# Kernel tuning notes

Measured on AMD Instinct MI355X. Metric: run time of the kernel, lower is better.

Reference implementation:

```python
import jax, jax.numpy as jnp
import numpy as np

DN = ('NCHW', 'OIHW', 'NCHW')

def conv2d(x, w, pad):
    return jax.lax.conv_general_dilated(x, w, (1, 1), [(pad, pad), (pad, pad)], dimension_numbers=DN)

def conv_module(x, w, g, b):
    # Conv2d -> BN (inference-mode per-channel affine) -> ReLU
    pad = (w.shape[-1] - 1) // 2
    y = conv2d(x, w, pad)
    return jax.nn.relu(y * g[None, :, None, None] + b[None, :, None, None])

def seq_conv_module(x, w, g, b):
    # x: (T, B, C, H, W) -> apply ConvModule per frame by folding T into batch
    T, B, C, H, W = x.shape
    y = conv_module(x.reshape(T * B, C, H, W), w, g, b)
    return y.reshape(T, B, -1, H, W)

def setup_inputs() -> dict:
    key = jax.random.key(0)
    ks = jax.random.split(key, 32)
    Cin, Ck, Cv, Cout = 1024, 256, 512, 512
    T, B, H, W = 4, 1, 64, 64
    s = 0.02
    d = {}
    d['x'] = jax.random.normal(ks[0], (B, Cin, H, W), jnp.float32)
    d['seq'] = jax.random.normal(ks[1], (T, B, Cin, H, W), jnp.float32)
    def mk_cm(i, cin, cout, k):
        return (jax.random.normal(ks[i], (cout, cin, k, k), jnp.float32) * s,
                jnp.ones((cout,), jnp.float32),
                jnp.zeros((cout,), jnp.float32))
    d['wk1'], d['gk1'], d['bk1'] = mk_cm(2, Cin, Ck, 1)
    d['wk2'], d['gk2'], d['bk2'] = mk_cm(3, Ck, Ck, 3)
    d['wv1'], d['gv1'], d['bv1'] = mk_cm(4, Cin, Cv, 1)
    d['wv2'], d['gv2'], d['bv2'] = mk_cm(5, Cv, Cv, 3)
    d['wqk1'], d['gqk1'], d['bqk1'] = mk_cm(6, Cin, Ck, 1)
    d['wqk2'], d['gqk2'], d['bqk2'] = mk_cm(7, Ck, Ck, 3)
    d['wqv1'], d['gqv1'], d['bqv1'] = mk_cm(8, Cin, Cv, 1)
    d['wqv2'], d['gqv2'], d['bqv2'] = mk_cm(9, Cv, Cv, 3)
    d['wb'], d['gb'], d['bb'] = mk_cm(10, 2 * Cv, Cout, 3)
    return d

def reference(x, seq, wk1, gk1, bk1, wk2, gk2, bk2, wv1, gv1, bv1, wv2, gv2, bv2,
              wqk1, gqk1, bqk1, wqk2, gqk2, bqk2, wqv1, gqv1, bqv1, wqv2, gqv2, bqv2,
              wb, gb, bb):
    # memory key/value convs over the T reference frames
    mk = seq_conv_module(seq_conv_module(seq, wk1, gk1, bk1), wk2, gk2, bk2)  # (T,B,Ck,H,W)
    mv = seq_conv_module(seq_conv_module(seq, wv1, gv1, bv1), wv2, gv2, bv2)  # (T,B,Cv,H,W)
    # query key/value convs on current frame
    qk = conv_module(conv_module(x, wqk1, gqk1, bqk1), wqk2, gqk2, bqk2)      # (B,Ck,H,W)
    qv = conv_module(conv_module(x, wqv1, gqv1, bqv1), wqv2, gqv2, bqv2)      # (B,Cv,H,W)
    T, B, Ck, H, W = mk.shape
    Cv = mv.shape[2]
    mk = jnp.transpose(mk, (1, 2, 0, 3, 4)).reshape(B, Ck, T * H * W)         # (B,Ck,THW)
    mv = jnp.transpose(mv, (1, 2, 0, 3, 4)).reshape(B, Cv, T * H * W)         # (B,Cv,THW)
    qkf = qk.reshape(B, Ck, H * W)                                            # (B,Ck,HW)
    # attention: (B,HW,THW); matmul_norm=False so no 1/sqrt(Ck) scaling
    attn = jax.nn.softmax(jnp.einsum('bcq,bck->bqk', qkf, mk), axis=-1)
    mem = jnp.einsum('bqk,bck->bcq', attn, mv).reshape(B, Cv, H, W)
    out = conv_module(jnp.concatenate([qv, mem], axis=1), wb, gb, bb)
    return out
```

## Files before the change

### kernel.cpp

```cpp
#include <hip/hip_runtime.h>
#include <stdint.h>


typedef short bf16x8 __attribute__((ext_vector_type(8)));
typedef float f32x4  __attribute__((ext_vector_type(4)));
typedef unsigned short u16x4 __attribute__((ext_vector_type(4)));

__device__ __forceinline__ unsigned short f2bf(float f) {
  union { float f; unsigned u; } x; x.f = f;
  unsigned r = x.u + 0x7FFFu + ((x.u >> 16) & 1u);
  return (unsigned short)(r >> 16);
}

typedef const __attribute__((address_space(1))) char* as1cp;
typedef __attribute__((address_space(3))) char* as3p;

__device__ __forceinline__ void gl_lds16(const char* g, char* l) {
  __builtin_amdgcn_global_load_lds((as1cp)g, (as3p)l, 16, 0, 0);
}

enum { EP_CL_BNR = 0, EP_CF_BNR_BF16 = 1, EP_CF_BNR_F32 = 2, EP_EXPSUM = 3,
       EP_PVDIV = 4, EP_PART = 5 };

template<int EP, bool CF, bool CONV3, bool XTILED>
__global__ __launch_bounds__(256) void gemm_k(
    const unsigned short* __restrict__ Wp,
    const unsigned short* __restrict__ Xp,
    int K, int Kc, int Xstride, int Xcoloff, int cin_log2,
    void* __restrict__ Op, int Ostride, int Ocoloff, size_t plane,
    const float* __restrict__ g1, const float* __restrict__ b1,
    const float* __restrict__ g2, const float* __restrict__ b2, int gsplit,
    float* __restrict__ rowsum, const char* __restrict__ zp)
{
  __shared__ short Wt[2][128 * 32];
  __shared__ short Xt[2][128 * 32];
  const int tid = threadIdx.x;
  const int w = tid >> 6;
  const int l = tid & 63;
  const int m0 = blockIdx.y * 128;
  const int n0 = blockIdx.x * 128;
  const int wrow0 = CF ? n0 : m0;
  const int xrow0 = CF ? m0 : n0;

  const int ch0 = w, ch1 = w + 4;
  const int sr0 = ch0 * 16 + (l >> 2);
  const int sr1 = ch1 * 16 + (l >> 2);
  const int kbp = (l & 3) << 4;
  const int kbl0 = kbp ^ ((sr0 & 3) << 4);
  const int kbl1 = kbp ^ ((sr1 & 3) << 4);

  const size_t wrb = (size_t)K * 2;
  const size_t xrb = (size_t)Xstride * 2;

  const int wm = (w >> 1) * 64;
  const int wn = (w & 1) * 64;

  const int k_begin = blockIdx.z * Kc;
  const int k_end = (k_begin + Kc < K) ? (k_begin + Kc) : K;

  auto stage = [&](int b, int k0) {
    int ci0 = k0, kh = 1, kw = 1, dpos = 0;
    if (CONV3) {
      int e = k0 >> cin_log2;
      ci0 = k0 & ((1 << cin_log2) - 1);
      kh = e / 3; kw = e - kh * 3;
      dpos = (kh - 1) * 64 + (kw - 1);
    }
    char* Wl = (char*)&Wt[b][0];
    char* Xl = (char*)&Xt[b][0];
    gl_lds16((const char*)Wp + (size_t)(wrow0 + sr0) * wrb + (size_t)k0 * 2 + kbl0,
             Wl + ch0 * 1024);
    gl_lds16((const char*)Wp + (size_t)(wrow0 + sr1) * wrb + (size_t)k0 * 2 + kbl1,
             Wl + ch1 * 1024);
    const char* xs0;
    const char* xs1;
    if constexpr (XTILED) {
      size_t kslab = (size_t)(k0 >> 5) * ((size_t)Xstride * 64);
      xs0 = (const char*)Xp + kslab + (size_t)(xrow0 + sr0) * 64 + kbl0;
      xs1 = (const char*)Xp + kslab + (size_t)(xrow0 + sr1) * 64 + kbl1;
    } else if constexpr (CONV3) {
      int p = xrow0 + sr0;
      int hw = p & 4095;
      int h2 = (hw >> 6) + kh - 1, w2 = (hw & 63) + kw - 1;
      xs0 = ((unsigned)h2 < 64u && (unsigned)w2 < 64u)
          ? (const char*)Xp + (size_t)(p + dpos) * xrb + (size_t)(Xcoloff + ci0) * 2 + kbl0
          : zp + kbl0;
      p = xrow0 + sr1;
      hw = p & 4095;
      h2 = (hw >> 6) + kh - 1; w2 = (hw & 63) + kw - 1;
      xs1 = ((unsigned)h2 < 64u && (unsigned)w2 < 64u)
          ? (const char*)Xp + (size_t)(p + dpos) * xrb + (size_t)(Xcoloff + ci0) * 2 + kbl1
          : zp + kbl1;
    } else {
      xs0 = (const char*)Xp + (size_t)(xrow0 + sr0) * xrb + (size_t)(Xcoloff + k0) * 2 + kbl0;
      xs1 = (const char*)Xp + (size_t)(xrow0 + sr1) * xrb + (size_t)(Xcoloff + k0) * 2 + kbl1;
    }
    gl_lds16(xs0, Xl + ch0 * 1024);
    gl_lds16(xs1, Xl + ch1 * 1024);
  };

  f32x4 acc[4][4] = {};

  int cur = 0;
  stage(0, k_begin);
  for (int k0 = k_begin; k0 < k_end; k0 += 32) {
    if (k0 + 32 < k_end) {
      stage(cur ^ 1, k0 + 32);
      asm volatile("s_waitcnt vmcnt(4)" ::: "memory");
    } else {
      asm volatile("s_waitcnt vmcnt(0)" ::: "memory");
    }
    __builtin_amdgcn_s_barrier();

    const short* Wb = &Wt[cur][0];
    const short* Xb = &Xt[cur][0];
    const short* At = CF ? Xb : Wb;
    const short* Bt = CF ? Wb : Xb;

    bf16x8 af[4], bfv[4];
#pragma unroll
    for (int i = 0; i < 4; i++) {
      int row = wm + i * 16 + (l & 15);
      int kb = ((l >> 4) << 4) ^ ((row & 3) << 4);
      af[i] = *(const bf16x8*)(At + row * 32 + (kb >> 1));
    }
#pragma unroll
    for (int j = 0; j < 4; j++) {
      int row = wn + j * 16 + (l & 15);
      int kb = ((l >> 4) << 4) ^ ((row & 3) << 4);
      bfv[j] = *(const bf16x8*)(Bt + row * 32 + (kb >> 1));
    }
#pragma unroll
    for (int i = 0; i < 4; i++)
#pragma unroll
      for (int j = 0; j < 4; j++)
        acc[i][j] = __builtin_amdgcn_mfma_f32_16x16x32_bf16(af[i], bfv[j], acc[i][j], 0, 0, 0);

    __builtin_amdgcn_s_barrier();
    cur ^= 1;
  }

  const int col = l & 15;
  const int rb = (l >> 4) << 2;

  if constexpr (EP == EP_PART) {
    float* P = (float*)Op + (size_t)blockIdx.z * plane;
#pragma unroll
    for (int j = 0; j < 4; j++) {
      int gn = n0 + wn + j * 16 + col;
#pragma unroll
      for (int i = 0; i < 4; i++) {
        int gm = m0 + wm + i * 16 + rb;
        *(f32x4*)(P + (size_t)gn * Ostride + gm) = acc[i][j];
      }
    }
  }
  if constexpr (EP == EP_CL_BNR) {
#pragma unroll
    for (int i = 0; i < 4; i++) {
      int gm = m0 + wm + i * 16 + rb;
      const float* gp; const float* bp;
      if (gm < gsplit) { gp = g1 + gm; bp = b1 + gm; }
      else             { gp = g2 + (gm - gsplit); bp = b2 + (gm - gsplit); }
      float G[4], B[4];
#pragma unroll
      for (int r = 0; r < 4; r++) { G[r] = gp[r]; B[r] = bp[r]; }
#pragma unroll
      for (int j = 0; j < 4; j++) {
        int gn = n0 + wn + j * 16 + col;
        f32x4 v = acc[i][j];
        u16x4 o;
#pragma unroll
        for (int r = 0; r < 4; r++) o[r] = f2bf(fmaxf(v[r] * G[r] + B[r], 0.f));
        *(u16x4*)((unsigned short*)Op + (size_t)gn * Ostride + Ocoloff + gm) = o;
      }
    }
  }
  if constexpr (EP == EP_CF_BNR_BF16 || EP == EP_CF_BNR_F32) {
#pragma unroll
    for (int j = 0; j < 4; j++) {
      int gn = n0 + wn + j * 16 + col;
      float G = (gn < gsplit) ? g1[gn] : g2[gn - gsplit];
      float Bv = (gn < gsplit) ? b1[gn] : b2[gn - gsplit];
#pragma unroll
      for (int i = 0; i < 4; i++) {
        int gm = m0 + wm + i * 16 + rb;
        f32x4 v = acc[i][j];
        if constexpr (EP == EP_CF_BNR_F32) {
          f32x4 o;
#pragma unroll
          for (int r = 0; r < 4; r++) o[r] = fmaxf(v[r] * G + Bv, 0.f);
          *(f32x4*)((float*)Op + (size_t)gn * Ostride + Ocoloff + gm) = o;
        } else {
          u16x4 o;
#pragma unroll
          for (int r = 0; r < 4; r++) o[r] = f2bf(fmaxf(v[r] * G + Bv, 0.f));
          *(u16x4*)((unsigned short*)Op + (size_t)gn * Ostride + Ocoloff + gm) = o;
        }
      }
    }
  }
  if constexpr (EP == EP_EXPSUM) {
#pragma unroll
    for (int j = 0; j < 4; j++) {
      int gn = n0 + wn + j * 16 + col;
      float s = 0.f;
#pragma unroll
      for (int i = 0; i < 4; i++) {
        int gm = m0 + wm + i * 16 + rb;
        f32x4 v = acc[i][j];
        u16x4 o;
#pragma unroll
        for (int r = 0; r < 4; r++) { float e = __expf(v[r]); s += e; o[r] = f2bf(e); }
        if (gsplit)
          *(u16x4*)((unsigned short*)Op + (size_t)(gm >> 5) * ((size_t)Ostride * 32)
                    + (size_t)gn * 32 + (gm & 31)) = o;
        else
          *(u16x4*)((unsigned short*)Op + (size_t)gn * Ostride + gm) = o;
      }
      s += __shfl_xor(s, 16);
      s += __shfl_xor(s, 32);
      if (l < 16) atomicAdd(rowsum + gn, s);
    }
  }
  if constexpr (EP == EP_PVDIV) {
#pragma unroll
    for (int j = 0; j < 4; j++) {
      int gn = n0 + wn + j * 16 + col;
      float inv = 1.0f / rowsum[gn];
#pragma unroll
      for (int i = 0; i < 4; i++) {
        int gm = m0 + wm + i * 16 + rb;
        f32x4 v = acc[i][j];
        u16x4 o;
#pragma unroll
        for (int r = 0; r < 4; r++) o[r] = f2bf(v[r] * inv);
        *(u16x4*)((unsigned short*)Op + (size_t)gn * Ostride + Ocoloff + gm) = o;
      }
    }
  }
}

enum { RED_BNR_BF16 = 0, RED_PVDIV = 1, RED_BNR_F32 = 2, RED_BNR_BF16_N = 3 };

template<int MODE>
__global__ __launch_bounds__(256) void reduce_k(
    const float* __restrict__ P, int Z, size_t plane, int Cdim,
    void* __restrict__ out, int Ostride, int Ocoloff,
    const float* __restrict__ g1, const float* __restrict__ b1,
    const float* __restrict__ g2, const float* __restrict__ b2, int gsplit,
    const float* __restrict__ rowsum, int total4)
{
  int t = blockIdx.x * 256 + threadIdx.x;
  if (t >= total4) return;
  size_t base = (size_t)t * 4;
  int n = (int)(base / (size_t)Cdim);
  int c = (int)(base % (size_t)Cdim);
  f32x4 s = *(const f32x4*)(P + base);
  for (int z = 1; z < Z; z++) {
    f32x4 v = *(const f32x4*)(P + (size_t)z * plane + base);
    s += v;
  }
  if constexpr (MODE == RED_BNR_BF16) {
    u16x4 o;
#pragma unroll
    for (int r = 0; r < 4; r++) {
      int ch = c + r;
      float G = (ch < gsplit) ? g1[ch] : g2[ch - gsplit];
      float B = (ch < gsplit) ? b1[ch] : b2[ch - gsplit];
      o[r] = f2bf(fmaxf(s[r] * G + B, 0.f));
    }
    *(u16x4*)((unsigned short*)out + (size_t)n * Ostride + Ocoloff + c) = o;
  }
  if constexpr (MODE == RED_BNR_BF16_N) {
    float G = g1[n], B = b1[n];
    u16x4 o;
#pragma unroll
    for (int r = 0; r < 4; r++) o[r] = f2bf(fmaxf(s[r] * G + B, 0.f));
    *(u16x4*)((unsigned short*)out + (size_t)n * Ostride + Ocoloff + c) = o;
  }
  if constexpr (MODE == RED_PVDIV) {
    float inv = 1.0f / rowsum[n];
    u16x4 o;
#pragma unroll
    for (int r = 0; r < 4; r++) o[r] = f2bf(s[r] * inv);
    *(u16x4*)((unsigned short*)out + (size_t)n * Ostride + Ocoloff + c) = o;
  }
  if constexpr (MODE == RED_BNR_F32) {
    float G = g1[n], B = b1[n];
    f32x4 o;
#pragma unroll
    for (int r = 0; r < 4; r++) o[r] = fmaxf(s[r] * G + B, 0.f);
    *(f32x4*)((float*)out + (size_t)n * Ostride + c) = o;
  }
}

__global__ __launch_bounds__(256) void nchw_to_cl(const float* __restrict__ src,
                                                  unsigned short* __restrict__ dst,
                                                  int C, int P) {
  __shared__ float t[32][33];
  int f = blockIdx.z;
  src += (size_t)f * C * P;
  dst += (size_t)f * C * P;
  int p0 = blockIdx.x * 32, c0 = blockIdx.y * 32;
  int a = threadIdx.x & 31, b = threadIdx.x >> 5;
#pragma unroll
  for (int k = 0; k < 4; k++)
    t[b + 8 * k][a] = src[(size_t)(c0 + b + 8 * k) * P + p0 + a];
  __syncthreads();
#pragma unroll
  for (int k = 0; k < 4; k++)
    dst[(size_t)(p0 + b + 8 * k) * C + c0 + a] = f2bf(t[a][b + 8 * k]);
}

__global__ __launch_bounds__(256) void cvt_bf16(const float* __restrict__ s,
                                                unsigned short* __restrict__ d, int n) {
  int i = blockIdx.x * 256 + threadIdx.x;
  if (i < n) d[i] = f2bf(s[i]);
}

__global__ __launch_bounds__(256) void repack3(const float* __restrict__ s,
                                               unsigned short* __restrict__ d,
                                               int ci_log2, int n) {
  int i = blockIdx.x * 256 + threadIdx.x;
  if (i >= n) return;
  int Ci = 1 << ci_log2;
  int ci = i & (Ci - 1);
  int t = i >> ci_log2;
  int e = t % 9;
  int co = t / 9;
  d[i] = f2bf(s[((size_t)co * Ci + ci) * 9 + e]);
}

__global__ __launch_bounds__(256) void fillf(float* p, float v, int n) {
  int i = blockIdx.x * 256 + threadIdx.x;
  if (i < n) p[i] = v;
}

extern "C" void kernel_launch(void* const* d_in, const int* in_sizes, int n_in,
                              void* d_out, int out_size, void* d_ws, size_t ws_size,
                              hipStream_t stream) {
  (void)in_sizes; (void)n_in;
  const float* x    = (const float*)d_in[0];
  const float* seq  = (const float*)d_in[1];
  const float* wk1  = (const float*)d_in[2];
  const float* gk1  = (const float*)d_in[3];
  const float* bk1  = (const float*)d_in[4];
  const float* wk2  = (const float*)d_in[5];
  const float* gk2  = (const float*)d_in[6];
  const float* bk2  = (const float*)d_in[7];
  const float* wv1  = (const float*)d_in[8];
  const float* gv1  = (const float*)d_in[9];
  const float* bv1  = (const float*)d_in[10];
  const float* wv2  = (const float*)d_in[11];
  const float* gv2  = (const float*)d_in[12];
  const float* bv2  = (const float*)d_in[13];
  const float* wqk1 = (const float*)d_in[14];
  const float* gqk1 = (const float*)d_in[15];
  const float* bqk1 = (const float*)d_in[16];
  const float* wqk2 = (const float*)d_in[17];
  const float* gqk2 = (const float*)d_in[18];
  const float* bqk2 = (const float*)d_in[19];
  const float* wqv1 = (const float*)d_in[20];
  const float* gqv1 = (const float*)d_in[21];
  const float* bqv1 = (const float*)d_in[22];
  const float* wqv2 = (const float*)d_in[23];
  const float* gqv2 = (const float*)d_in[24];
  const float* bqv2 = (const float*)d_in[25];
  const float* wb   = (const float*)d_in[26];
  const float* gb   = (const float*)d_in[27];
  const float* bb   = (const float*)d_in[28];

  char* ws = (char*)d_ws;
  size_t off = 0;
  auto alloc = [&](size_t bytes) { size_t o = off; off += (bytes + 255) & ~(size_t)255; return o; };
  size_t o_zp    = alloc(4096);
  size_t o_rs    = alloc(4096 * 4);
  size_t o_wKV1  = alloc((size_t)768 * 1024 * 2);
  size_t o_wQKV1 = alloc((size_t)768 * 1024 * 2);
  size_t o_wK2   = alloc((size_t)256 * 2304 * 2);
  size_t o_wQK2  = alloc((size_t)256 * 2304 * 2);
  size_t o_wV2   = alloc((size_t)512 * 4608 * 2);
  size_t o_wQV2  = alloc((size_t)512 * 4608 * 2);
  size_t o_wB    = alloc((size_t)512 * 9216 * 2);
  size_t o_mk    = alloc((size_t)16384 * 256 * 2);
  size_t o_mv    = alloc((size_t)512 * 16384 * 2);
  size_t o_qk    = alloc((size_t)4096 * 256 * 2);
  size_t o_qvm   = alloc((size_t)4096 * 1024 * 2);
  size_t o_part  = alloc((size_t)8 * 4096 * 512 * 4);
  size_t o_vol   = off;
  size_t o_xT    = o_vol;
  size_t o_seqT  = o_xT + (size_t)4096 * 1024 * 2;
  size_t o_kv1   = o_seqT + (size_t)4 * 4096 * 1024 * 2;
  size_t o_qkv1  = o_kv1 + (size_t)16384 * 768 * 2;
  size_t end1    = o_qkv1 + (size_t)4096 * 768 * 2;
  size_t o_expS  = o_vol;
  size_t end2    = o_expS + (size_t)4096 * 16384 * 2;
  size_t need    = end1 > end2 ? end1 : end2;

  bool SPLIT = ws_size >= need;
  if (!SPLIT) {
    size_t save = o_part;
    o_vol  = save;
    o_xT   = o_vol;
    o_seqT = o_xT + (size_t)4096 * 1024 * 2;
    o_kv1  = o_seqT + (size_t)4 * 4096 * 1024 * 2;
    o_qkv1 = o_kv1 + (size_t)16384 * 768 * 2;
    end1   = o_qkv1 + (size_t)4096 * 768 * 2;
    o_expS = o_vol;
    end2   = o_expS + (size_t)4096 * 16384 * 2;
    need   = end1 > end2 ? end1 : end2;
    if (ws_size < need) {
      fillf<<<(out_size + 255) / 256, 256, 0, stream>>>((float*)d_out, 12345.0f, out_size);
      return;
    }
  }

  const char* zp = ws + o_zp;
  float* rs = (float*)(ws + o_rs);
  unsigned short* wKV1p  = (unsigned short*)(ws + o_wKV1);
  unsigned short* wQKV1p = (unsigned short*)(ws + o_wQKV1);
  unsigned short* wK2p   = (unsigned short*)(ws + o_wK2);
  unsigned short* wQK2p  = (unsigned short*)(ws + o_wQK2);
  unsigned short* wV2p   = (unsigned short*)(ws + o_wV2);
  unsigned short* wQV2p  = (unsigned short*)(ws + o_wQV2);
  unsigned short* wBp    = (unsigned short*)(ws + o_wB);
  unsigned short* mkp    = (unsigned short*)(ws + o_mk);
  unsigned short* mvp    = (unsigned short*)(ws + o_mv);
  unsigned short* qkp    = (unsigned short*)(ws + o_qk);
  unsigned short* qvmp   = (unsigned short*)(ws + o_qvm);
  float* partp           = (float*)(ws + o_part);
  unsigned short* xTp    = (unsigned short*)(ws + o_xT);
  unsigned short* seqTp  = (unsigned short*)(ws + o_seqT);
  unsigned short* kv1p   = (unsigned short*)(ws + o_kv1);
  unsigned short* qkv1p  = (unsigned short*)(ws + o_qkv1);
  unsigned short* expSp  = (unsigned short*)(ws + o_expS);

  hipMemsetAsync(ws + o_zp, 0, 4096, stream);
  hipMemsetAsync(ws + o_rs, 0, 4096 * 4, stream);

  cvt_bf16<<<(256 * 1024 + 255) / 256, 256, 0, stream>>>(wk1, wKV1p, 256 * 1024);
  cvt_bf16<<<(512 * 1024 + 255) / 256, 256, 0, stream>>>(wv1, wKV1p + 256 * 1024, 512 * 1024);
  cvt_bf16<<<(256 * 1024 + 255) / 256, 256, 0, stream>>>(wqk1, wQKV1p, 256 * 1024);
  cvt_bf16<<<(512 * 1024 + 255) / 256, 256, 0, stream>>>(wqv1, wQKV1p + 256 * 1024, 512 * 1024);
  repack3<<<(256 * 2304 + 255) / 256, 256, 0, stream>>>(wk2, wK2p, 8, 256 * 2304);
  repack3<<<(256 * 2304 + 255) / 256, 256, 0, stream>>>(wqk2, wQK2p, 8, 256 * 2304);
  repack3<<<(512 * 4608 + 255) / 256, 256, 0, stream>>>(wv2, wV2p, 9, 512 * 4608);
  repack3<<<(512 * 4608 + 255) / 256, 256, 0, stream>>>(wqv2, wQV2p, 9, 512 * 4608);
  repack3<<<(512 * 9216 + 255) / 256, 256, 0, stream>>>(wb, wBp, 10, 512 * 9216);

  nchw_to_cl<<<dim3(128, 32, 1), 256, 0, stream>>>(x, xTp, 1024, 4096);
  nchw_to_cl<<<dim3(128, 32, 4), 256, 0, stream>>>(seq, seqTp, 1024, 4096);

  gemm_k<EP_CL_BNR, false, false, false><<<dim3(128, 6), 256, 0, stream>>>(
      wKV1p, seqTp, 1024, 1024, 1024, 0, 0, kv1p, 768, 0, 0,
      gk1, bk1, gv1, bv1, 256, rs, zp);

  if (SPLIT) {
    {
      size_t plane = (size_t)4096 * 768;
      gemm_k<EP_PART, false, false, false><<<dim3(32, 6, 4), 256, 0, stream>>>(
          wQKV1p, xTp, 1024, 256, 1024, 0, 0, partp, 768, 0, plane,
          nullptr, nullptr, nullptr, nullptr, 0, rs, zp);
      int t4 = (int)(plane / 4);
      reduce_k<RED_BNR_BF16><<<(t4 + 255) / 256, 256, 0, stream>>>(
          partp, 4, plane, 768, qkv1p, 768, 0, gqk1, bqk1, gqv1, bqv1, 256, rs, t4);
    }
    {
      size_t plane = (size_t)16384 * 256;
      gemm_k<EP_PART, false, true, false><<<dim3(128, 2, 4), 256, 0, stream>>>(
          wK2p, kv1p, 2304, 576, 768, 0, 8, partp, 256, 0, plane,
          nullptr, nullptr, nullptr, nullptr, 0, rs, zp);
      int t4 = (int)(plane / 4);
      reduce_k<RED_BNR_BF16><<<(t4 + 255) / 256, 256, 0, stream>>>(
          partp, 4, plane, 256, mkp, 256, 0, gk2, bk2, gk2, bk2, 256, rs, t4);
    }
    {
      size_t plane = (size_t)4096 * 256;
      gemm_k<EP_PART, false, true, false><<<dim3(32, 2, 8), 256, 0, stream>>>(
          wQK2p, qkv1p, 2304, 288, 768, 0, 8, partp, 256, 0, plane,
          nullptr, nullptr, nullptr, nullptr, 0, rs, zp);
      int t4 = (int)(plane / 4);
      reduce_k<RED_BNR_BF16><<<(t4 + 255) / 256, 256, 0, stream>>>(
          partp, 8, plane, 256, qkp, 256, 0, gqk2, bqk2, gqk2, bqk2, 256, rs, t4);
    }
    {
      size_t plane = (size_t)4096 * 512;
      gemm_k<EP_PART, false, true, false><<<dim3(32, 4, 8), 256, 0, stream>>>(
          wQV2p, qkv1p, 4608, 576, 768, 256, 9, partp, 512, 0, plane,
          nullptr, nullptr, nullptr, nullptr, 0, rs, zp);
      int t4 = (int)(plane / 4);
      reduce_k<RED_BNR_BF16><<<(t4 + 255) / 256, 256, 0, stream>>>(
          partp, 8, plane, 512, qvmp, 1024, 0, gqv2, bqv2, gqv2, bqv2, 512, rs, t4);
    }
    {
      size_t plane = (size_t)512 * 16384;
      gemm_k<EP_PART, true, true, false><<<dim3(4, 128, 2), 256, 0, stream>>>(
          wV2p, kv1p, 4608, 2304, 768, 256, 9, partp, 16384, 0, plane,
          nullptr, nullptr, nullptr, nullptr, 0, rs, zp);
      int t4 = (int)(plane / 4);
      reduce_k<RED_BNR_BF16_N><<<(t4 + 255) / 256, 256, 0, stream>>>(
          partp, 2, plane, 16384, mvp, 16384, 0, gv2, bv2, nullptr, nullptr, 0, rs, t4);
    }
    gemm_k<EP_EXPSUM, false, false, false><<<dim3(32, 128), 256, 0, stream>>>(
        mkp, qkp, 256, 256, 256, 0, 0, expSp, 4096, 0, 0,
        nullptr, nullptr, nullptr, nullptr, 1, rs, zp);
    {
      size_t plane = (size_t)4096 * 512;
      gemm_k<EP_PART, false, false, true><<<dim3(32, 4, 8), 256, 0, stream>>>(
          mvp, expSp, 16384, 2048, 4096, 0, 0, partp, 512, 0, plane,
          nullptr, nullptr, nullptr, nullptr, 0, rs, zp);
      int t4 = (int)(plane / 4);
      reduce_k<RED_PVDIV><<<(t4 + 255) / 256, 256, 0, stream>>>(
          partp, 8, plane, 512, qvmp, 1024, 512, nullptr, nullptr, nullptr, nullptr, 0, rs, t4);
    }
    {
      size_t plane = (size_t)512 * 4096;
      gemm_k<EP_PART, true, true, false><<<dim3(4, 32, 8), 256, 0, stream>>>(
          wBp, qvmp, 9216, 1152, 1024, 0, 10, partp, 4096, 0, plane,
          nullptr, nullptr, nullptr, nullptr, 0, rs, zp);
      int t4 = (int)(plane / 4);
      reduce_k<RED_BNR_F32><<<(t4 + 255) / 256, 256, 0, stream>>>(
          partp, 8, plane, 4096, (float*)d_out, 4096, 0, gb, bb, gb, bb, 512, rs, t4);
    }
  } else {
    gemm_k<EP_CL_BNR, false, false, false><<<dim3(32, 6), 256, 0, stream>>>(
        wQKV1p, xTp, 1024, 1024, 1024, 0, 0, qkv1p, 768, 0, 0,
        gqk1, bqk1, gqv1, bqv1, 256, rs, zp);
    gemm_k<EP_CL_BNR, false, true, false><<<dim3(128, 2), 256, 0, stream>>>(
        wK2p, kv1p, 2304, 2304, 768, 0, 8, mkp, 256, 0, 0,
        gk2, bk2, gk2, bk2, 256, rs, zp);
    gemm_k<EP_CL_BNR, false, true, false><<<dim3(32, 2), 256, 0, stream>>>(
        wQK2p, qkv1p, 2304, 2304, 768, 0, 8, qkp, 256, 0, 0,
        gqk2, bqk2, gqk2, bqk2, 256, rs, zp);
    gemm_k<EP_CL_BNR, false, true, false><<<dim3(32, 4), 256, 0, stream>>>(
        wQV2p, qkv1p, 4608, 4608, 768, 256, 9, qvmp, 1024, 0, 0,
        gqv2, bqv2, gqv2, bqv2, 512, rs, zp);
    gemm_k<EP_CF_BNR_BF16, true, true, false><<<dim3(4, 128), 256, 0, stream>>>(
        wV2p, kv1p, 4608, 4608, 768, 256, 9, mvp, 16384, 0, 0,
        gv2, bv2, gv2, bv2, 512, rs, zp);
    gemm_k<EP_EXPSUM, false, false, false><<<dim3(32, 128), 256, 0, stream>>>(
        mkp, qkp, 256, 256, 256, 0, 0, expSp, 16384, 0, 0,
        nullptr, nullptr, nullptr, nullptr, 0, rs, zp);
    gemm_k<EP_PVDIV, false, false, false><<<dim3(32, 4), 256, 0, stream>>>(
        mvp, expSp, 16384, 16384, 16384, 0, 0, qvmp, 1024, 512, 0,
        nullptr, nullptr, nullptr, nullptr, 0, rs, zp);
    gemm_k<EP_CF_BNR_F32, true, true, false><<<dim3(4, 32), 256, 0, stream>>>(
        wBp, qvmp, 9216, 9216, 1024, 0, 10, (float*)d_out, 4096, 0, 0,
        gb, bb, gb, bb, 512, rs, zp);
  }
}
```

Before: 625.5 us.

## Add 256x256-tile 512-thread GEMM kernel for the large split-K partial GEMMs

Adds a new gemm256 kernel that uses 256x256 output tiles with 8 waves. It stages the K dimension in two 32-wide halves with double-buffered direct global-to-LDS loads, uses a swizzled LDS layout, and raises wave priority around the MFMA burst. Five of the partial-sum GEMMs (3x3 convs, the PV product, and the final conv) now run on it instead of the 128x128 gemm_k. The goal is more data reuse per LDS load and higher MFMA density. The cost is fewer blocks per launch and higher register pressure from 32 accumulators per thread.

```diff
diff --git a/kernel.cpp b/kernel.cpp
--- a/kernel.cpp
+++ b/kernel.cpp
@@ -17,6 +17,131 @@
 
 __device__ __forceinline__ void gl_lds16(const char* g, char* l) {
   __builtin_amdgcn_global_load_lds((as1cp)g, (as3p)l, 16, 0, 0);
+}
+
+template<bool CF, bool CONV3, bool XTILED>
+__global__ __launch_bounds__(512, 2) void gemm256(
+    const unsigned short* __restrict__ Wp,
+    const unsigned short* __restrict__ Xp,
+    int K, int Kc, int Xstride, int Xcoloff, int cin_log2,
+    float* __restrict__ P, int Mtot, size_t plane,
+    const char* __restrict__ zp)
+{
+  __shared__ short Ap[2][2][8192];
+  __shared__ short Bp[2][2][8192];
+  const int tid = threadIdx.x;
+  const int w = tid >> 6;
+  const int l = tid & 63;
+  const int wm_idx = w >> 2;
+  const int wn_idx = w & 3;
+  const int n0 = blockIdx.x * 256;
+  const int m0 = blockIdx.y * 256;
+  const int wrow0 = CF ? n0 : m0;
+  const int xrow0 = CF ? m0 : n0;
+
+  const int g = (l & 7) ^ (l >> 3);
+  const int grow0 = w * 32 + 2 * (l >> 3) + (g >> 2);
+  const int gc = g & 3;
+
+  auto srcW = [&](int grow, int h, int k0) -> const char* {
+    return (const char*)Wp +
+           (((size_t)(wrow0 + grow)) * K + (size_t)(k0 + h * 32 + gc * 8)) * 2;
+  };
+  auto srcX = [&](int grow, int h, int k0) -> const char* {
+    if constexpr (XTILED) {
+      return (const char*)Xp + (size_t)((k0 + h * 32) >> 5) * ((size_t)Xstride * 64)
+             + (size_t)(xrow0 + grow) * 64 + gc * 16;
+    } else if constexpr (CONV3) {
+      int e = k0 >> cin_log2;
+      int ci0 = k0 & ((1 << cin_log2) - 1);
+      int kh = e / 3, kw = e - kh * 3;
+      int dpos = (kh - 1) * 64 + (kw - 1);
+      int p = xrow0 + grow;
+      int hw = p & 4095;
+      int h2 = (hw >> 6) + kh - 1, w2 = (hw & 63) + kw - 1;
+      return ((unsigned)h2 < 64u && (unsigned)w2 < 64u)
+          ? (const char*)Xp + (((size_t)(p + dpos)) * Xstride
+                               + (size_t)(Xcoloff + ci0 + h * 32 + gc * 8)) * 2
+          : zp + gc * 16;
+    } else {
+      return (const char*)Xp + (((size_t)(xrow0 + grow)) * Xstride
+                                + (size_t)(Xcoloff + k0 + h * 32 + gc * 8)) * 2;
+    }
+  };
+
+  auto stage_half = [&](int b, int h, int k0) {
+#pragma unroll
+    for (int j = 0; j < 2; j++) {
+      int grow = grow0 + j * 16;
+      const char* sm = CF ? srcX(grow, h, k0) : srcW(grow, h, k0);
+      gl_lds16(sm, (char*)&Ap[b][h][0] + w * 2048 + j * 1024);
+    }
+#pragma unroll
+    for (int j = 0; j < 2; j++) {
+      int grow = grow0 + j * 16;
+      const char* sn = CF ? srcW(grow, h, k0) : srcX(grow, h, k0);
+      gl_lds16(sn, (char*)&Bp[b][h][0] + w * 2048 + j * 1024);
+    }
+  };
+
+  auto rd = [&](const short* base, int row, int ks) -> bf16x8 {
+    int R = row >> 1;
+    int sp = (((row & 1) << 2) | ks) ^ (R & 7);
+    return *(const bf16x8*)(base + R * 64 + sp * 8);
+  };
+
+  f32x4 acc[8][4] = {};
+
+  const int kb = blockIdx.z * Kc;
+  const int NT = Kc >> 6;
+
+  stage_half(0, 0, kb);
+  stage_half(0, 1, kb);
+  asm volatile("s_waitcnt vmcnt(4)" ::: "memory");
+  __builtin_amdgcn_s_barrier();
+
+  int buf = 0;
+  for (int t = 0; t < NT; ++t) {
+    int k0n = kb + (t + 1) * 64;
+    bool pre = (t + 1 < NT);
+#pragma unroll
+    for (int h = 0; h < 2; ++h) {
+      const short* Am = &Ap[buf][h][0];
+      const short* Bm = &Bp[buf][h][0];
+      bf16x8 af[8], bfv[4];
+#pragma unroll
+      for (int i = 0; i < 8; i++)
+        af[i] = rd(Am, wm_idx * 128 + i * 16 + (l & 15), l >> 4);
+#pragma unroll
+      for (int j = 0; j < 4; j++)
+        bfv[j] = rd(Bm, wn_idx * 64 + j * 16 + (l & 15), l >> 4);
+      if (pre) stage_half(buf ^ 1, h, k0n);
+      __builtin_amdgcn_s_setprio(1);
+#pragma unroll
+      for (int i = 0; i < 8; i++)
+#pragma unroll
+        for (int j = 0; j < 4; j++)
+          acc[i][j] = __builtin_amdgcn_mfma_f32_16x16x32_bf16(af[i], bfv[j], acc[i][j], 0, 0, 0);
+      __builtin_amdgcn_s_setprio(0);
+      if (pre) asm volatile("s_waitcnt vmcnt(4)" ::: "memory");
+      else     asm volatile("s_waitcnt vmcnt(0)" ::: "memory");
+      __builtin_amdgcn_s_barrier();
+    }
+    buf ^= 1;
+  }
+
+  float* Pz = P + (size_t)blockIdx.z * plane;
+  const int col = l & 15;
+  const int rb2 = (l >> 4) << 2;
+#pragma unroll
+  for (int j = 0; j < 4; j++) {
+    int gn = n0 + wn_idx * 64 + j * 16 + col;
+#pragma unroll
+    for (int i = 0; i < 8; i++) {
+      int gm = m0 + wm_idx * 128 + i * 16 + rb2;
+      *(f32x4*)(Pz + (size_t)gn * Mtot + gm) = acc[i][j];
+    }
+  }
 }
 
 enum { EP_CL_BNR = 0, EP_CF_BNR_BF16 = 1, EP_CF_BNR_F32 = 2, EP_EXPSUM = 3,
@@ -468,9 +593,8 @@
     }
     {
       size_t plane = (size_t)16384 * 256;
-      gemm_k<EP_PART, false, true, false><<<dim3(128, 2, 4), 256, 0, stream>>>(
-          wK2p, kv1p, 2304, 576, 768, 0, 8, partp, 256, 0, plane,
-          nullptr, nullptr, nullptr, nullptr, 0, rs, zp);
+      gemm256<false, true, false><<<dim3(64, 1, 4), 512, 0, stream>>>(
+          wK2p, kv1p, 2304, 576, 768, 0, 8, partp, 256, plane, zp);
       int t4 = (int)(plane / 4);
       reduce_k<RED_BNR_BF16><<<(t4 + 255) / 256, 256, 0, stream>>>(
           partp, 4, plane, 256, mkp, 256, 0, gk2, bk2, gk2, bk2, 256, rs, t4);
@@ -486,18 +610,16 @@
     }
     {
       size_t plane = (size_t)4096 * 512;
-      gemm_k<EP_PART, false, true, false><<<dim3(32, 4, 8), 256, 0, stream>>>(
-          wQV2p, qkv1p, 4608, 576, 768, 256, 9, partp, 512, 0, plane,
-          nullptr, nullptr, nullptr, nullptr, 0, rs, zp);
+      gemm256<false, true, false><<<dim3(16, 2, 8), 512, 0, stream>>>(
+          wQV2p, qkv1p, 4608, 576, 768, 256, 9, partp, 512, plane, zp);
       int t4 = (int)(plane / 4);
       reduce_k<RED_BNR_BF16><<<(t4 + 255) / 256, 256, 0, stream>>>(
           partp, 8, plane, 512, qvmp, 1024, 0, gqv2, bqv2, gqv2, bqv2, 512, rs, t4);
     }
     {
       size_t plane = (size_t)512 * 16384;
-      gemm_k<EP_PART, true, true, false><<<dim3(4, 128, 2), 256, 0, stream>>>(
-          wV2p, kv1p, 4608, 2304, 768, 256, 9, partp, 16384, 0, plane,
-          nullptr, nullptr, nullptr, nullptr, 0, rs, zp);
+      gemm256<true, true, false><<<dim3(2, 64, 2), 512, 0, stream>>>(
+          wV2p, kv1p, 4608, 2304, 768, 256, 9, partp, 16384, plane, zp);
       int t4 = (int)(plane / 4);
       reduce_k<RED_BNR_BF16_N><<<(t4 + 255) / 256, 256, 0, stream>>>(
           partp, 2, plane, 16384, mvp, 16384, 0, gv2, bv2, nullptr, nullptr, 0, rs, t4);
@@ -507,18 +629,16 @@
         nullptr, nullptr, nullptr, nullptr, 1, rs, zp);
     {
       size_t plane = (size_t)4096 * 512;
-      gemm_k<EP_PART, false, false, true><<<dim3(32, 4, 8), 256, 0, stream>>>(
-          mvp, expSp, 16384, 2048, 4096, 0, 0, partp, 512, 0, plane,
-          nullptr, nullptr, nullptr, nullptr, 0, rs, zp);
+      gemm256<false, false, true><<<dim3(16, 2, 8), 512, 0, stream>>>(
+          mvp, expSp, 16384, 2048, 4096, 0, 0, partp, 512, plane, zp);
       int t4 = (int)(plane / 4);
       reduce_k<RED_PVDIV><<<(t4 + 255) / 256, 256, 0, stream>>>(
           partp, 8, plane, 512, qvmp, 1024, 512, nullptr, nullptr, nullptr, nullptr, 0, rs, t4);
     }
     {
       size_t plane = (size_t)512 * 4096;
-      gemm_k<EP_PART, true, true, false><<<dim3(4, 32, 8), 256, 0, stream>>>(
-          wBp, qvmp, 9216, 1152, 1024, 0, 10, partp, 4096, 0, plane,
-          nullptr, nullptr, nullptr, nullptr, 0, rs, zp);
+      gemm256<true, true, false><<<dim3(2, 16, 8), 512, 0, stream>>>(
+          wBp, qvmp, 9216, 1152, 1024, 0, 10, partp, 4096, plane, zp);
       int t4 = (int)(plane / 4);
       reduce_k<RED_BNR_F32><<<(t4 + 255) / 256, 256, 0, stream>>>(
           partp, 8, plane, 4096, (float*)d_out, 4096, 0, gb, bb, gb, bb, 512, rs, t4);
```

New measurement: 564.8 us. 1.11x faster.
